# Performance work log

Measured on AMD Instinct MI355X. Metric: run time of the kernel, lower is better.

## Reference

```python
import jax, jax.numpy as jnp
import numpy as np

B, S, IN, H, OUT = 64, 512, 1024, 512, 512
EPS = 1e-5
ADAPTIVE_RATE = 0.01


def setup_inputs() -> dict:
    key = jax.random.key(0)
    ks = iter(jax.random.split(key, 64))

    def rn(shape, scale):
        return (jax.random.normal(next(ks), shape, jnp.float32) * scale)

    d = {}
    d["x"] = jax.random.normal(next(ks), (B, S, IN), jnp.float32)
    d["context"] = jax.random.normal(next(ks), (B, H), jnp.float32)
    d["state_importance"] = jnp.ones((1, H), jnp.float32)
    # embedding
    d["W_emb"], d["b_emb"] = rn((H, IN), 0.02), rn((H,), 0.01)
    # core layers: Linear + BatchNorm1d (gamma=1, beta=0 torch init)
    d["W0"], d["b0"] = rn((H, H), 0.03), rn((H,), 0.01)
    d["g0"], d["bt0"] = jnp.ones((H,), jnp.float32), jnp.zeros((H,), jnp.float32)
    d["W1"], d["b1"] = rn((H, H), 0.03), rn((H,), 0.01)
    d["g1"], d["bt1"] = jnp.ones((H,), jnp.float32), jnp.zeros((H,), jnp.float32)
    # two LSTMCells (hidden -> hidden), torch gate order i,f,g,o
    lstm_scale = 1.0 / np.sqrt(H)
    for l in range(2):
        d[f"Wih{l}"] = rn((4 * H, H), lstm_scale)
        d[f"Whh{l}"] = rn((4 * H, H), lstm_scale)
        d[f"bih{l}"] = rn((4 * H,), lstm_scale)
        d[f"bhh{l}"] = rn((4 * H,), lstm_scale)
    # compression gate: Linear(2H, H) + LayerNorm + Sigmoid
    d["Wc"], d["bc"] = rn((H, 2 * H), 0.02), rn((H,), 0.01)
    d["lnc_g"], d["lnc_b"] = jnp.ones((H,), jnp.float32), jnp.zeros((H,), jnp.float32)
    # importance generator: Linear, ReLU, Linear, LayerNorm, Sigmoid
    d["Wi1"], d["bi1"] = rn((H, H), 0.03), rn((H,), 0.01)
    d["Wi2"], d["bi2"] = rn((H, H), 0.03), rn((H,), 0.01)
    d["lni_g"], d["lni_b"] = jnp.ones((H,), jnp.float32), jnp.zeros((H,), jnp.float32)
    # final layer
    d["Wf"], d["bf"] = rn((OUT, H), 0.03), rn((OUT,), 0.01)
    return d


def _bn_channel_dim1(h, gamma, beta):
    # BatchNorm1d (training mode) on (B, S, H) with channel dim = dim 1 (S == num_features)
    m = h.mean(axis=(0, 2), keepdims=True)
    v = h.var(axis=(0, 2), keepdims=True)  # biased, like torch normalization
    return gamma[None, :, None] * (h - m) / jnp.sqrt(v + EPS) + beta[None, :, None]


def _ln(h, g, b):
    m = h.mean(-1, keepdims=True)
    v = h.var(-1, keepdims=True)
    return g * (h - m) / jnp.sqrt(v + EPS) + b


def _lstm_cell(xt, h, c, Wih, Whh, bih, bhh):
    z = xt @ Wih.T + bih + h @ Whh.T + bhh  # (B, 4H)
    i, f, g, o = jnp.split(z, 4, axis=-1)
    c = jax.nn.sigmoid(f) * c + jax.nn.sigmoid(i) * jnp.tanh(g)
    h = jax.nn.sigmoid(o) * jnp.tanh(c)
    return h, c


def reference(x, context, state_importance, W_emb, b_emb,
              W0, b0, g0, bt0, W1, b1, g1, bt1,
              Wih0, Whh0, bih0, bhh0, Wih1, Whh1, bih1, bhh1,
              Wc, bc, lnc_g, lnc_b, Wi1, bi1, Wi2, bi2, lni_g, lni_b,
              Wf, bf):
    h = x @ W_emb.T + b_emb  # (B, S, H)
    h = jax.nn.relu(_bn_channel_dim1(h @ W0.T + b0, g0, bt0))
    h = jax.nn.relu(_bn_channel_dim1(h @ W1.T + b1, g1, bt1))

    # stacked 2-layer LSTMCell over the sequence, keep only the final hidden
    zeros = jnp.zeros((B, H), h.dtype)

    def step(carry, xt):
        h0, c0, h1, c1 = carry
        h0, c0 = _lstm_cell(xt, h0, c0, Wih0, Whh0, bih0, bhh0)
        h1, c1 = _lstm_cell(h0, h1, c1, Wih1, Whh1, bih1, bhh1)
        return (h0, c0, h1, c1), None

    (h0, c0, h1, c1), _ = jax.lax.scan(step, (zeros, zeros, zeros, zeros),
                                       jnp.swapaxes(h, 0, 1))
    processed = h1  # (B, H)

    comp = jax.nn.sigmoid(_ln(jnp.concatenate([processed, context], axis=-1) @ Wc.T + bc,
                              lnc_g, lnc_b))
    compressed = processed * comp

    imp = jax.nn.sigmoid(_ln(jax.nn.relu(compressed @ Wi1.T + bi1) @ Wi2.T + bi2,
                             lni_g, lni_b))
    si_new = state_importance + ADAPTIVE_RATE * (
        jnp.abs(imp).mean(axis=0, keepdims=True) - state_importance)

    out = compressed @ Wf.T + bf
    return out, si_new
```

## Files before the change

### kernel.cpp

```cpp
#include <hip/hip_runtime.h>
#include <hip/hip_bf16.h>
#include <stdint.h>


typedef __attribute__((ext_vector_type(8))) short short8;
typedef __attribute__((ext_vector_type(4))) float floatx4;
typedef __attribute__((ext_vector_type(4))) unsigned uintx4;

__device__ inline float b2f(short u){
  union { float f; uint32_t i; } x; x.i = ((uint32_t)(uint16_t)u) << 16; return x.f;
}
__device__ inline short f2b(float f){
  union { float f; uint32_t i; } x; x.f = f;
  uint32_t r = (x.i + 0x7FFFu + ((x.i >> 16) & 1u)) >> 16;
  return (short)(uint16_t)r;
}
__device__ inline float sigm(float x){ return 1.0f / (1.0f + __expf(-x)); }

__device__ inline float blk_sum(float v, float* red){
  #pragma unroll
  for (int o = 32; o > 0; o >>= 1) v += __shfl_down(v, o, 64);
  int wv = threadIdx.x >> 6;
  __syncthreads();
  if ((threadIdx.x & 63) == 0) red[wv] = v;
  __syncthreads();
  return red[0] + red[1] + red[2] + red[3];
}

__device__ inline void stage16(const short* g, short* l){
  __builtin_amdgcn_global_load_lds(
      (const __attribute__((address_space(1))) void*)(uintptr_t)g,
      (__attribute__((address_space(3))) void*)(uintptr_t)l,
      16, 0, 0);
}


__global__ void set_flag(const unsigned* __restrict__ si_bits, unsigned* __restrict__ flag){
  if (threadIdx.x == 0 && blockIdx.x == 0)
    *flag = (si_bits[0] == 0x3F800000u) ? 1u : 0u;
}


__global__ __launch_bounds__(256) void convq(
    const unsigned* __restrict__ flag, int mode,
    const void* s0, long e0, short* d0, int n0,
    const void* s1, long e1, short* d1, int n1,
    const void* s2, long e2, short* d2, int n2,
    const void* s3, long e3, short* d3, int n3)
{
  const bool isf32 = (*flag != 0u);
  const int gid = blockIdx.x*256 + threadIdx.x;
  const int stride = gridDim.x*256;
  const void* ss[4] = {s0,s1,s2,s3};
  long ee[4]  = {e0,e1,e2,e3};
  short* dd[4] = {d0,d1,d2,d3};
  int nn[4]   = {n0,n1,n2,n3};
  for (int s = 0; s < 4; s++){
    if (!dd[s]) continue;
    if (mode == 1) {
      if (!isf32) continue;
      for (int i = gid; i < nn[s]; i += stride)
        dd[s][i] = ((const short*)ss[s])[ee[s] + i];
    } else if (isf32) {
      for (int i = gid; i < nn[s]; i += stride)
        dd[s][i] = f2b(((const float*)ss[s])[ee[s] + i]);
    } else {
      for (int i = gid; i < nn[s]; i += stride)
        dd[s][i] = ((const short*)ss[s])[ee[s] + i];
    }
  }
}


__global__ __launch_bounds__(256) void gemm_bt(
    const short* __restrict__ A, const short* __restrict__ A2, int splitRow,
    int lda, const short* __restrict__ W, const short* __restrict__ bias,
    short* __restrict__ C, int ldc, int row0, int K)
{
  __shared__ alignas(16) short As[128*32];
  __shared__ alignas(16) short Bs[128*32];
  const int tid  = threadIdx.x;
  const int lane = tid & 63;
  const int wave = tid >> 6;
  const int wm = wave >> 1, wn = wave & 1;
  const int bm = blockIdx.x, bn = blockIdx.y;
  const int R0 = row0 + bm*128;
  const short* Ab = (R0 < splitRow) ? A2 : A;

  floatx4 acc[4][4];
  #pragma unroll
  for (int i = 0; i < 4; i++)
    #pragma unroll
    for (int j = 0; j < 4; j++){ floatx4 z = {0.f,0.f,0.f,0.f}; acc[i][j] = z; }

  const short* Ag = Ab + (size_t)(R0 + (tid >> 2))*lda + (tid & 3)*8;
  const short* Wg = W  + (size_t)(bn*128 + (tid >> 2))*K + (tid & 3)*8;

  const int kk  = (lane >> 4) * 8;
  const int rA  = wm*64 + (lane & 15);
  const int rB  = wn*64 + (lane & 15);

  for (int k0 = 0; k0 < K; k0 += 32) {
    __syncthreads();
    stage16(Ag + k0,                  As + tid*8);
    stage16(Ag + k0 + (size_t)64*lda, As + 2048 + tid*8);
    stage16(Wg + k0,                  Bs + tid*8);
    stage16(Wg + k0 + (size_t)64*K,   Bs + 2048 + tid*8);
    __syncthreads();

    short8 af[4], bf[4];
    #pragma unroll
    for (int i = 0; i < 4; i++){
      af[i] = *(const short8*)&As[(rA + i*16)*32 + kk];
      bf[i] = *(const short8*)&Bs[(rB + i*16)*32 + kk];
    }
    #pragma unroll
    for (int i = 0; i < 4; i++)
      #pragma unroll
      for (int j = 0; j < 4; j++)
        acc[i][j] = __builtin_amdgcn_mfma_f32_16x16x32_bf16(af[i], bf[j], acc[i][j], 0, 0, 0);
  }

  const int crow0 = R0 + wm*64 + (lane >> 4)*4;
  const int ccol0 = bn*128 + wn*64;
  #pragma unroll
  for (int i = 0; i < 4; i++){
    #pragma unroll
    for (int j = 0; j < 4; j++){
      int col = ccol0 + j*16 + (lane & 15);
      float bv = b2f(bias[col]);
      #pragma unroll
      for (int r = 0; r < 4; r++){
        int row = crow0 + i*16 + r;
        C[(size_t)row*ldc + col] = f2b(acc[i][j][r] + bv);
      }
    }
  }
}


__global__ __launch_bounds__(256) void bn_relu(
    const short* __restrict__ X, const short* __restrict__ gamma,
    const short* __restrict__ beta, short* __restrict__ Y)
{
  const int s = blockIdx.x, tid = threadIdx.x;
  __shared__ float red[4];
  float s1 = 0.f, s2 = 0.f;
  for (int i = tid; i < 4096; i += 256){
    int b = i >> 6, c = i & 63;
    short8 v = *(const short8*)(X + ((size_t)(b*512 + s))*512 + c*8);
    #pragma unroll
    for (int u = 0; u < 8; u++){ float f = b2f(v[u]); s1 += f; s2 += f*f; }
  }
  s1 = blk_sum(s1, red);
  s2 = blk_sum(s2, red);
  float mean = s1 * (1.f/32768.f);
  float var  = fmaxf(s2 * (1.f/32768.f) - mean*mean, 0.f);
  float sc = b2f(gamma[s]) * rsqrtf(var + 1e-5f);
  float sh = b2f(beta[s]) - mean * sc;
  for (int i = tid; i < 4096; i += 256){
    int b = i >> 6, c = i & 63;
    size_t base = ((size_t)(b*512 + s))*512 + c*8;
    short8 v = *(const short8*)(X + base);
    short8 o;
    #pragma unroll
    for (int u = 0; u < 8; u++){
      float f = b2f(v[u]) * sc + sh;
      o[u] = f2b(fmaxf(f, 0.f));
    }
    *(short8*)(Y + base) = o;
  }
}


__global__ __launch_bounds__(256, 1) void lstm_persist(
    const short* __restrict__ Xseq,
    const short* __restrict__ Wih0, const short* __restrict__ Whh0,
    const short* __restrict__ bih0, const short* __restrict__ bhh0,
    const short* __restrict__ Wih1, const short* __restrict__ Whh1,
    const short* __restrict__ bih1, const short* __restrict__ bhh1,
    short* __restrict__ h0r,
    short* __restrict__ h1r,
    unsigned* __restrict__ slots,
    unsigned* __restrict__ epoch)
{
  const int wg   = blockIdx.x;
  const int tid  = threadIdx.x;
  const int lane = tid & 63;
  const int wave = tid >> 6;

  if (wg == 64){
    if (wave != 0) return;
    const unsigned* sp = slots + lane*16;
    unsigned* ep = epoch + lane*16;
    for (unsigned itv = 1; itv <= 512; ++itv){
      for (;;){
        unsigned v;
        asm volatile("global_load_dword %0, %1, off sc1\n\t"
                     "s_waitcnt vmcnt(0)"
                     : "=v"(v) : "v"(sp) : "memory");
        if (__all((int)(v >= itv))) break;
      }
      asm volatile("global_store_dword %0, %1, off sc0 sc1"
                   :: "v"(ep), "v"(itv) : "memory");
    }
    return;
  }

  const int l15  = lane & 15;
  const int quad = lane >> 4;
  const int kq   = quad * 8;

  __shared__ float zp[4*64*33];
  __shared__ unsigned pack[2][256];
  __shared__ alignas(16) short xpf[512];
  #define ZP(t,r,c) zp[((t)*64 + (r))*33 + (c)]

  const short* Wt = (wave==0) ? Wih0 : (wave==1) ? Whh0 : (wave==2) ? Wih1 : Whh1;
  short8 wreg[2][16];
  #pragma unroll
  for (int nt = 0; nt < 2; nt++){
    int g2 = nt*2 + (l15 >> 3);
    int ml = l15 & 7;
    const short* wrow = Wt + (size_t)(g2*512 + wg*8 + ml)*512 + kq;
    #pragma unroll
    for (int kk = 0; kk < 16; kk++)
      wreg[nt][kk] = *(const short8*)(wrow + kk*32);
  }

  const int bb  = tid >> 2;
  const int ml0 = (tid & 3) * 2;
  float bs0[4][2], bs1[4][2];
  #pragma unroll
  for (int g = 0; g < 4; g++)
    #pragma unroll
    for (int p = 0; p < 2; p++){
      int m = wg*8 + ml0 + p;
      bs0[g][p] = b2f(bih0[g*512+m]) + b2f(bhh0[g*512+m]);
      bs1[g][p] = b2f(bih1[g*512+m]) + b2f(bhh1[g*512+m]);
    }
  float c0[2] = {0.f, 0.f}, c1[2] = {0.f, 0.f};

  for (int it = 0; it <= 512; ++it){
    const bool act = (wave==0) ? (it < 512)
                   : (wave==1) ? (it >= 1 && it < 512)
                   : (wave==2) ? (it >= 1)
                   :             (it >= 2);

    if (it > 0 && wave > 0 && act){
      const unsigned want = (unsigned)it;
      const unsigned* ep = epoch + wg*16;
      for (;;){
        unsigned v;
        asm volatile("global_load_dword %0, %1, off sc1\n\t"
                     "s_waitcnt vmcnt(0)"
                     : "=v"(v) : "v"(ep) : "memory");
        if (v >= want) break;
      }
      __builtin_amdgcn_sched_barrier(0);
    }

    floatx4 acc[4][2];
    #pragma unroll
    for (int mt = 0; mt < 4; mt++)
      #pragma unroll
      for (int nt = 0; nt < 2; nt++){ floatx4 z = {0.f,0.f,0.f,0.f}; acc[mt][nt] = z; }

    if (act){
      const short* Ab;
      size_t rstride;
      if (wave == 0)      { Ab = Xseq + (size_t)it*512;               rstride = 262144; }
      else if (wave <= 2) { Ab = h0r + (size_t)((it-1)&1)*32768;      rstride = 512; }
      else                { Ab = h1r + (size_t)(it&1)*32768;          rstride = 512; }
      const short* ap[4];
      #pragma unroll
      for (int mt = 0; mt < 4; mt++)
        ap[mt] = Ab + (size_t)(mt*16 + l15)*rstride + kq;

      if (wave == 0){
        #pragma unroll
        for (int kk = 0; kk < 16; kk++){
          short8 af[4];
          #pragma unroll
          for (int mt = 0; mt < 4; mt++) af[mt] = *(const short8*)(ap[mt] + kk*32);
          #pragma unroll
          for (int mt = 0; mt < 4; mt++){
            acc[mt][0] = __builtin_amdgcn_mfma_f32_16x16x32_bf16(af[mt], wreg[0][kk], acc[mt][0], 0, 0, 0);
            acc[mt][1] = __builtin_amdgcn_mfma_f32_16x16x32_bf16(af[mt], wreg[1][kk], acc[mt][1], 0, 0, 0);
          }
        }
      } else {
        short8 hb[2][4][4];
        #pragma unroll
        for (int pb = 0; pb < 2; pb++)
          #pragma unroll
          for (int kk = 0; kk < 4; kk++)
            #pragma unroll
            for (int mt = 0; mt < 4; mt++)
              asm volatile("global_load_dwordx4 %0, %1, off sc1"
                           : "=v"(hb[pb][kk][mt])
                           : "v"(ap[mt] + (pb*4 + kk)*32));
        #pragma unroll
        for (int kb = 0; kb < 4; kb++){
          const int cur = kb & 1;
          if (kb < 3) asm volatile("s_waitcnt vmcnt(16)" ::: "memory");
          else        asm volatile("s_waitcnt vmcnt(0)"  ::: "memory");
          __builtin_amdgcn_sched_barrier(0);
          #pragma unroll
          for (int kk = 0; kk < 4; kk++)
            #pragma unroll
            for (int mt = 0; mt < 4; mt++){
              acc[mt][0] = __builtin_amdgcn_mfma_f32_16x16x32_bf16(hb[cur][kk][mt], wreg[0][kb*4+kk], acc[mt][0], 0, 0, 0);
              acc[mt][1] = __builtin_amdgcn_mfma_f32_16x16x32_bf16(hb[cur][kk][mt], wreg[1][kb*4+kk], acc[mt][1], 0, 0, 0);
            }
          if (kb < 2){
            #pragma unroll
            for (int kk = 0; kk < 4; kk++)
              #pragma unroll
              for (int mt = 0; mt < 4; mt++)
                asm volatile("global_load_dwordx4 %0, %1, off sc1"
                             : "=v"(hb[cur][kk][mt])
                             : "v"(ap[mt] + ((kb+2)*4 + kk)*32));
          }
        }
      }
    }

    #pragma unroll
    for (int mt = 0; mt < 4; mt++)
      #pragma unroll
      for (int nt = 0; nt < 2; nt++)
        #pragma unroll
        for (int r = 0; r < 4; r++)
          ZP(wave, mt*16 + quad*4 + r, nt*16 + l15) = acc[mt][nt][r];
    __syncthreads();

    if (it < 512){
      float hv[2];
      #pragma unroll
      for (int p = 0; p < 2; p++){
        int ml = ml0 + p;
        float zi = ZP(0, bb,      ml) + ZP(1, bb,      ml) + bs0[0][p];
        float zf = ZP(0, bb,  8 + ml) + ZP(1, bb,  8 + ml) + bs0[1][p];
        float zg = ZP(0, bb, 16 + ml) + ZP(1, bb, 16 + ml) + bs0[2][p];
        float zo = ZP(0, bb, 24 + ml) + ZP(1, bb, 24 + ml) + bs0[3][p];
        c0[p] = sigm(zf)*c0[p] + sigm(zi)*tanhf(zg);
        hv[p] = sigm(zo)*tanhf(c0[p]);
      }
      pack[0][tid] = (unsigned)(uint16_t)f2b(hv[0]) | ((unsigned)(uint16_t)f2b(hv[1]) << 16);
    }
    if (it >= 1){
      float hv[2];
      #pragma unroll
      for (int p = 0; p < 2; p++){
        int ml = ml0 + p;
        float zi = ZP(2, bb,      ml) + ZP(3, bb,      ml) + bs1[0][p];
        float zf = ZP(2, bb,  8 + ml) + ZP(3, bb,  8 + ml) + bs1[1][p];
        float zg = ZP(2, bb, 16 + ml) + ZP(3, bb, 16 + ml) + bs1[2][p];
        float zo = ZP(2, bb, 24 + ml) + ZP(3, bb, 24 + ml) + bs1[3][p];
        c1[p] = sigm(zf)*c1[p] + sigm(zi)*tanhf(zg);
        hv[p] = sigm(zo)*tanhf(c1[p]);
      }
      pack[1][tid] = (unsigned)(uint16_t)f2b(hv[0]) | ((unsigned)(uint16_t)f2b(hv[1]) << 16);
    }
    __syncthreads();

    if (wave == 0 && it < 512){
      uintx4 d = *(const uintx4*)&pack[0][lane*4];
      short* dst = h0r + (size_t)(it&1)*32768 + lane*512 + wg*8;
      asm volatile("global_store_dwordx4 %0, %1, off sc0 sc1" :: "v"(dst), "v"(d) : "memory");
      asm volatile("s_waitcnt vmcnt(0)" ::: "memory");
    }
    if (wave == 1 && it >= 1){
      uintx4 d = *(const uintx4*)&pack[1][lane*4];
      short* dst = h1r + (size_t)((it-1)&1)*32768 + lane*512 + wg*8;
      asm volatile("global_store_dwordx4 %0, %1, off sc0 sc1" :: "v"(dst), "v"(d) : "memory");
      asm volatile("s_waitcnt vmcnt(0)" ::: "memory");
    }
    __syncthreads();
    if (tid == 0){
      unsigned nv = (unsigned)(it + 1);
      asm volatile("global_store_dword %0, %1, off sc0 sc1"
                   :: "v"(slots + wg*16), "v"(nv) : "memory");
    }
    if (wave == 0 && it + 2 < 512){
      const short* nx = Xseq + (size_t)(it + 2)*512 + lane*8;
      #pragma unroll 8
      for (int r = 0; r < 64; ++r)
        stage16(nx + (size_t)r*262144, xpf);
    }
  }
  #undef ZP
}


__global__ __launch_bounds__(256) void head_gate_out(
    const short* __restrict__ h1, const short* __restrict__ ctx,
    const short* __restrict__ Wc, const short* __restrict__ bc,
    const short* __restrict__ lng, const short* __restrict__ lnb,
    const short* __restrict__ Wf, const short* __restrict__ bfb,
    short* __restrict__ compressed, void* __restrict__ outp,
    const unsigned* __restrict__ flag)
{
  const int b = blockIdx.x, tid = threadIdx.x;
  const bool isf32 = (*flag != 0u);
  __shared__ float xc[1024];
  __shared__ float cv[512];
  __shared__ float red[4];
  for (int i = tid; i < 512; i += 256) xc[i]       = b2f(h1 [b*512 + i]);
  for (int i = tid; i < 512; i += 256) xc[512 + i] = b2f(ctx[b*512 + i]);
  __syncthreads();
  float y[2];
  #pragma unroll
  for (int jj = 0; jj < 2; jj++){
    int j = tid + jj*256;
    const short* wr = Wc + (size_t)j*1024;
    float a = 0.f;
    for (int k = 0; k < 1024; k += 8){
      short8 wv = *(const short8*)(wr + k);
      #pragma unroll
      for (int u = 0; u < 8; u++) a += b2f(wv[u]) * xc[k + u];
    }
    y[jj] = a + b2f(bc[j]);
  }
  float s = blk_sum(y[0] + y[1], red);
  float mean = s * (1.f/512.f);
  float q = (y[0]-mean)*(y[0]-mean) + (y[1]-mean)*(y[1]-mean);
  q = blk_sum(q, red);
  float inv = rsqrtf(q * (1.f/512.f) + 1e-5f);
  #pragma unroll
  for (int jj = 0; jj < 2; jj++){
    int j = tid + jj*256;
    float v = (y[jj]-mean)*inv*b2f(lng[j]) + b2f(lnb[j]);
    float cm = xc[j] * sigm(v);
    cv[j] = cm;
    compressed[(size_t)b*512 + j] = f2b(cm);
  }
  __syncthreads();
  #pragma unroll
  for (int jj = 0; jj < 2; jj++){
    int j = tid + jj*256;
    const short* wr = Wf + (size_t)j*512;
    float a = 0.f;
    for (int k = 0; k < 512; k += 8){
      short8 wv = *(const short8*)(wr + k);
      #pragma unroll
      for (int u = 0; u < 8; u++) a += b2f(wv[u]) * cv[k + u];
    }
    float o = a + b2f(bfb[j]);
    if (isf32) ((float*)outp)[(size_t)b*512 + j] = o;
    else       ((short*)outp)[(size_t)b*512 + j] = f2b(o);
  }
}


__global__ __launch_bounds__(256) void head_imp(
    const short* __restrict__ compressed,
    const short* __restrict__ Wi1, const short* __restrict__ bi1,
    const short* __restrict__ Wi2, const short* __restrict__ bi2,
    const short* __restrict__ lng, const short* __restrict__ lnb,
    float* __restrict__ imp)
{
  const int b = blockIdx.x, tid = threadIdx.x;
  __shared__ float xr[512];
  __shared__ float t1[512];
  __shared__ float red[4];
  for (int i = tid; i < 512; i += 256) xr[i] = b2f(compressed[b*512 + i]);
  __syncthreads();
  #pragma unroll
  for (int jj = 0; jj < 2; jj++){
    int j = tid + jj*256;
    const short* wr = Wi1 + (size_t)j*512;
    float a = 0.f;
    for (int k = 0; k < 512; k += 8){
      short8 wv = *(const short8*)(wr + k);
      #pragma unroll
      for (int u = 0; u < 8; u++) a += b2f(wv[u]) * xr[k + u];
    }
    t1[j] = fmaxf(a + b2f(bi1[j]), 0.f);
  }
  __syncthreads();
  float y[2];
  #pragma unroll
  for (int jj = 0; jj < 2; jj++){
    int j = tid + jj*256;
    const short* wr = Wi2 + (size_t)j*512;
    float a = 0.f;
    for (int k = 0; k < 512; k += 8){
      short8 wv = *(const short8*)(wr + k);
      #pragma unroll
      for (int u = 0; u < 8; u++) a += b2f(wv[u]) * t1[k + u];
    }
    y[jj] = a + b2f(bi2[j]);
  }
  float s = blk_sum(y[0] + y[1], red);
  float mean = s * (1.f/512.f);
  float q = (y[0]-mean)*(y[0]-mean) + (y[1]-mean)*(y[1]-mean);
  q = blk_sum(q, red);
  float inv = rsqrtf(q * (1.f/512.f) + 1e-5f);
  #pragma unroll
  for (int jj = 0; jj < 2; jj++){
    int j = tid + jj*256;
    imp[(size_t)b*512 + j] = sigm((y[jj]-mean)*inv*b2f(lng[j]) + b2f(lnb[j]));
  }
}


__global__ __launch_bounds__(256) void head_si(
    const float* __restrict__ imp, const short* __restrict__ si,
    void* __restrict__ outp, const unsigned* __restrict__ flag)
{
  int tid = threadIdx.x;
  const bool isf32 = (*flag != 0u);
  #pragma unroll
  for (int mm = 0; mm < 2; mm++){
    int m = tid + mm*256;
    float s = 0.f;
    for (int b = 0; b < 64; b++) s += fabsf(imp[(size_t)b*512 + m]);
    float mean = s * (1.f/64.f);
    float sv = b2f(si[m]);
    float o = sv + 0.01f*(mean - sv);
    if (isf32) ((float*)outp)[32768 + m] = o;
    else       ((short*)outp)[32768 + m] = f2b(o);
  }
}


extern "C" void kernel_launch(void* const* d_in, const int* in_sizes, int n_in,
                              void* d_out, int out_size, void* d_ws, size_t ws_size,
                              hipStream_t stream)
{
  (void)in_sizes; (void)n_in; (void)out_size; (void)ws_size;
  char* ws = (char*)d_ws;
  unsigned* slots  = (unsigned*)(ws);
  unsigned* epoch  = (unsigned*)(ws + 4096);
  unsigned* flag   = (unsigned*)(ws + 8192);
  short*    xStage = (short*)(ws + 12288);
  short*    ring   = (short*)(ws + 274432);
  short*    comp   = (short*)(ws + 798720);
  float*    impb   = (float*)(ws + 864256);
  short*    SA     = (short*)(ws + 995328);

  short* h0r = ring;
  short* h1r = ring + 65536;

  short* aWemb = SA + 0;
  short* aW0   = SA + 524288;
  short* aW1   = SA + 786432;
  short* aWih0 = SA + 1048576;
  short* aWhh0 = SA + 2097152;
  short* aWih1 = SA + 3145728;
  short* aWhh1 = SA + 4194304;
  short* aWc   = SA + 5242880;
  short* aWi1  = SA + 5767168;
  short* aWi2  = SA + 6029312;
  short* aWf   = SA + 6291456;
  short* V     = SA + 6553600;
  short* abemb = V + 0;     short* ab0  = V + 512;   short* ag0  = V + 1024;
  short* abt0  = V + 1536;  short* ab1  = V + 2048;  short* ag1  = V + 2560;
  short* abt1  = V + 3072;  short* abih0= V + 3584;  short* abhh0= V + 5632;
  short* abih1 = V + 7680;  short* abhh1= V + 9728;  short* abc  = V + 11776;
  short* alncg = V + 12288; short* alncb= V + 12800; short* abi1 = V + 13312;
  short* abi2  = V + 13824; short* alnig= V + 14336; short* alnib= V + 14848;
  short* abfb  = V + 15360; short* actx = V + 15872; short* asi  = V + 48640;

  short* xb  = (short*)d_in[0];
  short* hL0 = xb + 16777216;

  hipMemsetAsync(slots, 0, 8192, stream);
  set_flag<<<1, 64, 0, stream>>>((const unsigned*)d_in[2], flag);

  dim3 blk(256);
  convq<<<256, blk, 0, stream>>>(flag, 0,
      d_in[0], 0, xStage, 65536, nullptr,0,nullptr,0, nullptr,0,nullptr,0, nullptr,0,nullptr,0);
  for (long n0 = 65536; n0 < 33554432; n0 <<= 1) {
    int blocks = (int)((n0 + 1023) / 1024); if (blocks > 4096) blocks = 4096;
    convq<<<blocks, blk, 0, stream>>>(flag, 0,
        d_in[0], n0, xb + n0, (int)n0, nullptr,0,nullptr,0, nullptr,0,nullptr,0, nullptr,0,nullptr,0);
  }
  convq<<<64, blk, 0, stream>>>(flag, 1,
      xStage, 0, xb, 65536, nullptr,0,nullptr,0, nullptr,0,nullptr,0, nullptr,0,nullptr,0);

  convq<<<1024, blk, 0, stream>>>(flag, 0,
      d_in[3], 0, aWemb, 524288,  d_in[5], 0, aW0, 262144,
      d_in[9], 0, aW1,   262144,  d_in[21],0, aWc, 524288);
  convq<<<2048, blk, 0, stream>>>(flag, 0,
      d_in[13],0, aWih0, 1048576, d_in[14],0, aWhh0, 1048576,
      d_in[17],0, aWih1, 1048576, d_in[18],0, aWhh1, 1048576);
  convq<<<1024, blk, 0, stream>>>(flag, 0,
      d_in[25],0, aWi1, 262144,   d_in[27],0, aWi2, 262144,
      d_in[31],0, aWf,  262144,   d_in[1], 0, actx, 32768);
  convq<<<8, blk, 0, stream>>>(flag, 0,
      d_in[4], 0, abemb, 512,  d_in[6], 0, ab0, 512,
      d_in[7], 0, ag0,   512,  d_in[8], 0, abt0, 512);
  convq<<<8, blk, 0, stream>>>(flag, 0,
      d_in[10],0, ab1, 512,  d_in[11],0, ag1, 512,
      d_in[12],0, abt1,512,  d_in[22],0, abc, 512);
  convq<<<8, blk, 0, stream>>>(flag, 0,
      d_in[15],0, abih0, 2048,  d_in[16],0, abhh0, 2048,
      d_in[19],0, abih1, 2048,  d_in[20],0, abhh1, 2048);
  convq<<<8, blk, 0, stream>>>(flag, 0,
      d_in[23],0, alncg, 512,  d_in[24],0, alncb, 512,
      d_in[26],0, abi1,  512,  d_in[28],0, abi2,  512);
  convq<<<8, blk, 0, stream>>>(flag, 0,
      d_in[29],0, alnig, 512,  d_in[30],0, alnib, 512,
      d_in[32],0, abfb,  512,  d_in[2], 0, asi,   512);

  gemm_bt<<<dim3(1, 4), blk, 0, stream>>>(xb, xb, 0, 1024, aWemb, abemb,
                                          xStage, 512, 0, 1024);
  for (int r0 = 128; r0 < 32768; r0 <<= 1) {
    gemm_bt<<<dim3(r0/128, 4), blk, 0, stream>>>(xb, xb, 0, 1024, aWemb, abemb,
                                                 xb, 512, r0, 1024);
  }
  gemm_bt<<<dim3(256, 4), blk, 0, stream>>>(xb, xStage, 128, 512, aW0, ab0,
                                            hL0, 512, 0, 512);
  bn_relu<<<512, blk, 0, stream>>>(hL0, ag0, abt0, hL0);
  gemm_bt<<<dim3(256, 4), blk, 0, stream>>>(hL0, hL0, 0, 512, aW1, ab1,
                                            xb, 512, 0, 512);
  bn_relu<<<512, blk, 0, stream>>>(xb, ag1, abt1, xb);

  lstm_persist<<<65, blk, 0, stream>>>(xb, aWih0, aWhh0, abih0, abhh0,
                                       aWih1, aWhh1, abih1, abhh1,
                                       h0r, h1r, slots, epoch);

  head_gate_out<<<64, blk, 0, stream>>>(h1r + 32768, actx, aWc, abc, alncg, alncb,
                                        aWf, abfb, comp, d_out, flag);
  head_imp<<<64, blk, 0, stream>>>(comp, aWi1, abi1, aWi2, abi2, alnig, alnib, impb);
  head_si<<<1, blk, 0, stream>>>(impb, asi, d_out, flag);
}
```

Measured before the change: 7.044 ms.

## Split LSTM layer barriers into independent per-layer flags with LDS wave signaling

```diff
diff --git a/kernel.cpp b/kernel.cpp
--- a/kernel.cpp
+++ b/kernel.cpp
@@ -5,7 +5,7 @@
 
 typedef __attribute__((ext_vector_type(8))) short short8;
 typedef __attribute__((ext_vector_type(4))) float floatx4;
-typedef __attribute__((ext_vector_type(4))) unsigned uintx4;
+typedef __attribute__((ext_vector_type(2))) unsigned uintx2;
 
 __device__ inline float b2f(short u){
   union { float f; uint32_t i; } x; x.i = ((uint32_t)(uint16_t)u) << 16; return x.f;
@@ -32,6 +32,16 @@
       (const __attribute__((address_space(1))) void*)(uintptr_t)g,
       (__attribute__((address_space(3))) void*)(uintptr_t)l,
       16, 0, 0);
+}
+
+__device__ inline int ldsLoadAcq(int* p){
+  return __hip_atomic_load(p, __ATOMIC_ACQUIRE, __HIP_MEMORY_SCOPE_WORKGROUP);
+}
+__device__ inline void ldsStoreRel(int* p, int v){
+  __hip_atomic_store(p, v, __ATOMIC_RELEASE, __HIP_MEMORY_SCOPE_WORKGROUP);
+}
+__device__ inline int ldsAddRel(int* p){
+  return __hip_atomic_fetch_add(p, 1, __ATOMIC_RELEASE, __HIP_MEMORY_SCOPE_WORKGROUP);
 }
 
 
@@ -181,8 +191,10 @@
     const short* __restrict__ bih1, const short* __restrict__ bhh1,
     short* __restrict__ h0r,
     short* __restrict__ h1r,
-    unsigned* __restrict__ slots,
-    unsigned* __restrict__ epoch)
+    unsigned* __restrict__ f0,
+    unsigned* __restrict__ f1,
+    unsigned* __restrict__ ep0,
+    unsigned* __restrict__ ep1)
 {
   const int wg   = blockIdx.x;
   const int tid  = threadIdx.x;
@@ -190,9 +202,9 @@
   const int wave = tid >> 6;
 
   if (wg == 64){
-    if (wave != 0) return;
-    const unsigned* sp = slots + lane*16;
-    unsigned* ep = epoch + lane*16;
+    if (wave >= 2) return;
+    const unsigned* sp = (wave == 0 ? f0 : f1) + lane*16;
+    unsigned* dp = (wave == 0 ? ep0 : ep1) + lane*16;
     for (unsigned itv = 1; itv <= 512; ++itv){
       for (;;){
         unsigned v;
@@ -202,7 +214,7 @@
         if (__all((int)(v >= itv))) break;
       }
       asm volatile("global_store_dword %0, %1, off sc0 sc1"
-                   :: "v"(ep), "v"(itv) : "memory");
+                   :: "v"(dp), "v"(itv) : "memory");
     }
     return;
   }
@@ -211,10 +223,15 @@
   const int quad = lane >> 4;
   const int kq   = quad * 8;
 
-  __shared__ float zp[4*64*33];
-  __shared__ unsigned pack[2][256];
+  __shared__ float zp0[2*2*64*33];
+  __shared__ float zp1[2*2*64*33];
   __shared__ alignas(16) short xpf[512];
-  #define ZP(t,r,c) zp[((t)*64 + (r))*33 + (c)]
+  __shared__ int go0, go1, zc0, zc1, gc0, gc1;
+  #define ZPL0(p,t,r,c) zp0[((((p)*2+(t))*64) + (r))*33 + (c)]
+  #define ZPL1(p,t,r,c) zp1[((((p)*2+(t))*64) + (r))*33 + (c)]
+
+  if (tid == 0){ go0 = -1; go1 = -1; zc0 = 0; zc1 = 0; gc0 = 0; gc1 = 0; }
+  __syncthreads();
 
   const short* Wt = (wave==0) ? Wih0 : (wave==1) ? Whh0 : (wave==2) ? Wih1 : Whh1;
   short8 wreg[2][16];
@@ -228,18 +245,21 @@
       wreg[nt][kk] = *(const short8*)(wrow + kk*32);
   }
 
-  const int bb  = tid >> 2;
-  const int ml0 = (tid & 3) * 2;
-  float bs0[4][2], bs1[4][2];
+  const int lp  = wave >> 1;
+  const int t2  = tid & 127;
+  const int bbg = t2 >> 1;
+  const int m4  = (t2 & 1) * 4;
+  const short* biA = lp ? bih1 : bih0;
+  const short* bhA = lp ? bhh1 : bhh0;
+  float bsL[4][4];
   #pragma unroll
   for (int g = 0; g < 4; g++)
     #pragma unroll
-    for (int p = 0; p < 2; p++){
-      int m = wg*8 + ml0 + p;
-      bs0[g][p] = b2f(bih0[g*512+m]) + b2f(bhh0[g*512+m]);
-      bs1[g][p] = b2f(bih1[g*512+m]) + b2f(bhh1[g*512+m]);
-    }
-  float c0[2] = {0.f, 0.f}, c1[2] = {0.f, 0.f};
+    for (int j = 0; j < 4; j++){
+      int m = wg*8 + m4 + j;
+      bsL[g][j] = b2f(biA[g*512+m]) + b2f(bhA[g*512+m]);
+    }
+  float cst[4] = {0.f, 0.f, 0.f, 0.f};
 
   for (int it = 0; it <= 512; ++it){
     const bool act = (wave==0) ? (it < 512)
@@ -247,16 +267,36 @@
                    : (wave==2) ? (it >= 1)
                    :             (it >= 2);
 
-    if (it > 0 && wave > 0 && act){
+    if (wave == 1 && it >= 1){
       const unsigned want = (unsigned)it;
-      const unsigned* ep = epoch + wg*16;
+      const unsigned* p = ep0 + wg*16;
       for (;;){
         unsigned v;
         asm volatile("global_load_dword %0, %1, off sc1\n\t"
                      "s_waitcnt vmcnt(0)"
-                     : "=v"(v) : "v"(ep) : "memory");
+                     : "=v"(v) : "v"(p) : "memory");
         if (v >= want) break;
       }
+      __builtin_amdgcn_sched_barrier(0);
+      if (lane == 0) ldsStoreRel(&go0, it);
+    }
+    if (wave == 3){
+      if (it >= 2){
+        const unsigned want = (unsigned)it;
+        const unsigned* p = ep1 + wg*16;
+        for (;;){
+          unsigned v;
+          asm volatile("global_load_dword %0, %1, off sc1\n\t"
+                       "s_waitcnt vmcnt(0)"
+                       : "=v"(v) : "v"(p) : "memory");
+          if (v >= want) break;
+        }
+        __builtin_amdgcn_sched_barrier(0);
+      }
+      if (lane == 0) ldsStoreRel(&go1, it);
+    }
+    if (wave == 2 && it >= 1){
+      while (ldsLoadAcq(&go0) < it) { }
       __builtin_amdgcn_sched_barrier(0);
     }
 
@@ -326,71 +366,104 @@
       }
     }
 
-    #pragma unroll
-    for (int mt = 0; mt < 4; mt++)
-      #pragma unroll
-      for (int nt = 0; nt < 2; nt++)
+    const int par = it & 1;
+    if (wave < 2){
+      if (it < 512){
+        if (it >= 2) while (ldsLoadAcq(&gc0) < 2*(it-1)) { }
         #pragma unroll
-        for (int r = 0; r < 4; r++)
-          ZP(wave, mt*16 + quad*4 + r, nt*16 + l15) = acc[mt][nt][r];
-    __syncthreads();
-
-    if (it < 512){
-      float hv[2];
-      #pragma unroll
-      for (int p = 0; p < 2; p++){
-        int ml = ml0 + p;
-        float zi = ZP(0, bb,      ml) + ZP(1, bb,      ml) + bs0[0][p];
-        float zf = ZP(0, bb,  8 + ml) + ZP(1, bb,  8 + ml) + bs0[1][p];
-        float zg = ZP(0, bb, 16 + ml) + ZP(1, bb, 16 + ml) + bs0[2][p];
-        float zo = ZP(0, bb, 24 + ml) + ZP(1, bb, 24 + ml) + bs0[3][p];
-        c0[p] = sigm(zf)*c0[p] + sigm(zi)*tanhf(zg);
-        hv[p] = sigm(zo)*tanhf(c0[p]);
-      }
-      pack[0][tid] = (unsigned)(uint16_t)f2b(hv[0]) | ((unsigned)(uint16_t)f2b(hv[1]) << 16);
-    }
-    if (it >= 1){
-      float hv[2];
-      #pragma unroll
-      for (int p = 0; p < 2; p++){
-        int ml = ml0 + p;
-        float zi = ZP(2, bb,      ml) + ZP(3, bb,      ml) + bs1[0][p];
-        float zf = ZP(2, bb,  8 + ml) + ZP(3, bb,  8 + ml) + bs1[1][p];
-        float zg = ZP(2, bb, 16 + ml) + ZP(3, bb, 16 + ml) + bs1[2][p];
-        float zo = ZP(2, bb, 24 + ml) + ZP(3, bb, 24 + ml) + bs1[3][p];
-        c1[p] = sigm(zf)*c1[p] + sigm(zi)*tanhf(zg);
-        hv[p] = sigm(zo)*tanhf(c1[p]);
-      }
-      pack[1][tid] = (unsigned)(uint16_t)f2b(hv[0]) | ((unsigned)(uint16_t)f2b(hv[1]) << 16);
-    }
-    __syncthreads();
-
-    if (wave == 0 && it < 512){
-      uintx4 d = *(const uintx4*)&pack[0][lane*4];
-      short* dst = h0r + (size_t)(it&1)*32768 + lane*512 + wg*8;
-      asm volatile("global_store_dwordx4 %0, %1, off sc0 sc1" :: "v"(dst), "v"(d) : "memory");
-      asm volatile("s_waitcnt vmcnt(0)" ::: "memory");
-    }
-    if (wave == 1 && it >= 1){
-      uintx4 d = *(const uintx4*)&pack[1][lane*4];
-      short* dst = h1r + (size_t)((it-1)&1)*32768 + lane*512 + wg*8;
-      asm volatile("global_store_dwordx4 %0, %1, off sc0 sc1" :: "v"(dst), "v"(d) : "memory");
-      asm volatile("s_waitcnt vmcnt(0)" ::: "memory");
-    }
-    __syncthreads();
-    if (tid == 0){
-      unsigned nv = (unsigned)(it + 1);
-      asm volatile("global_store_dword %0, %1, off sc0 sc1"
-                   :: "v"(slots + wg*16), "v"(nv) : "memory");
-    }
-    if (wave == 0 && it + 2 < 512){
-      const short* nx = Xseq + (size_t)(it + 2)*512 + lane*8;
-      #pragma unroll 8
-      for (int r = 0; r < 64; ++r)
-        stage16(nx + (size_t)r*262144, xpf);
-    }
-  }
-  #undef ZP
+        for (int mt = 0; mt < 4; mt++)
+          #pragma unroll
+          for (int nt = 0; nt < 2; nt++)
+            #pragma unroll
+            for (int r = 0; r < 4; r++)
+              ZPL0(par, wave, mt*16 + quad*4 + r, nt*16 + l15) = acc[mt][nt][r];
+        if (lane == 0) ldsAddRel(&zc0);
+      }
+    } else {
+      if (it >= 1){
+        if (it >= 3) while (ldsLoadAcq(&gc1) < 2*(it-2)) { }
+        #pragma unroll
+        for (int mt = 0; mt < 4; mt++)
+          #pragma unroll
+          for (int nt = 0; nt < 2; nt++)
+            #pragma unroll
+            for (int r = 0; r < 4; r++)
+              ZPL1(par, wave-2, mt*16 + quad*4 + r, nt*16 + l15) = acc[mt][nt][r];
+        if (lane == 0) ldsAddRel(&zc1);
+      }
+    }
+
+    if (wave < 2){
+      if (it < 512){
+        while (ldsLoadAcq(&zc0) < 2*(it+1)) { }
+        if (it >= 2) while (ldsLoadAcq(&go1) < it) { }
+        float hv[4];
+        #pragma unroll
+        for (int j = 0; j < 4; j++){
+          int ml = m4 + j;
+          float zi = ZPL0(par,0,bbg,      ml) + ZPL0(par,1,bbg,      ml) + bsL[0][j];
+          float zf = ZPL0(par,0,bbg,  8 + ml) + ZPL0(par,1,bbg,  8 + ml) + bsL[1][j];
+          float zg = ZPL0(par,0,bbg, 16 + ml) + ZPL0(par,1,bbg, 16 + ml) + bsL[2][j];
+          float zo = ZPL0(par,0,bbg, 24 + ml) + ZPL0(par,1,bbg, 24 + ml) + bsL[3][j];
+          cst[j] = sigm(zf)*cst[j] + sigm(zi)*tanhf(zg);
+          hv[j] = sigm(zo)*tanhf(cst[j]);
+        }
+        uintx2 d;
+        d.x = (unsigned)(uint16_t)f2b(hv[0]) | ((unsigned)(uint16_t)f2b(hv[1]) << 16);
+        d.y = (unsigned)(uint16_t)f2b(hv[2]) | ((unsigned)(uint16_t)f2b(hv[3]) << 16);
+        short* dst = h0r + (size_t)par*32768 + bbg*512 + wg*8 + m4;
+        asm volatile("global_store_dwordx2 %0, %1, off sc0 sc1" :: "v"(dst), "v"(d) : "memory");
+        asm volatile("s_waitcnt vmcnt(0)" ::: "memory");
+        __builtin_amdgcn_sched_barrier(0);
+        if (lane == 0){
+          int old = ldsAddRel(&gc0);
+          if (old == 2*it + 1){
+            unsigned nv = (unsigned)(it + 1);
+            asm volatile("global_store_dword %0, %1, off sc0 sc1"
+                         :: "v"(f0 + wg*16), "v"(nv) : "memory");
+          }
+        }
+      }
+      if (wave == 0 && it + 2 < 512){
+        const short* nx = Xseq + (size_t)(it + 2)*512 + lane*8;
+        #pragma unroll 8
+        for (int r = 0; r < 64; ++r)
+          stage16(nx + (size_t)r*262144, xpf);
+      }
+    } else {
+      if (it >= 1){
+        while (ldsLoadAcq(&zc1) < 2*it) { }
+        float hv[4];
+        #pragma unroll
+        for (int j = 0; j < 4; j++){
+          int ml = m4 + j;
+          float zi = ZPL1(par,0,bbg,      ml) + ZPL1(par,1,bbg,      ml) + bsL[0][j];
+          float zf = ZPL1(par,0,bbg,  8 + ml) + ZPL1(par,1,bbg,  8 + ml) + bsL[1][j];
+          float zg = ZPL1(par,0,bbg, 16 + ml) + ZPL1(par,1,bbg, 16 + ml) + bsL[2][j];
+          float zo = ZPL1(par,0,bbg, 24 + ml) + ZPL1(par,1,bbg, 24 + ml) + bsL[3][j];
+          cst[j] = sigm(zf)*cst[j] + sigm(zi)*tanhf(zg);
+          hv[j] = sigm(zo)*tanhf(cst[j]);
+        }
+        uintx2 d;
+        d.x = (unsigned)(uint16_t)f2b(hv[0]) | ((unsigned)(uint16_t)f2b(hv[1]) << 16);
+        d.y = (unsigned)(uint16_t)f2b(hv[2]) | ((unsigned)(uint16_t)f2b(hv[3]) << 16);
+        short* dst = h1r + (size_t)((it-1)&1)*32768 + bbg*512 + wg*8 + m4;
+        asm volatile("global_store_dwordx2 %0, %1, off sc0 sc1" :: "v"(dst), "v"(d) : "memory");
+        asm volatile("s_waitcnt vmcnt(0)" ::: "memory");
+        __builtin_amdgcn_sched_barrier(0);
+        if (lane == 0){
+          int old = ldsAddRel(&gc1);
+          if (old == 2*it - 1){
+            unsigned nv = (unsigned)(it + 1);
+            asm volatile("global_store_dword %0, %1, off sc0 sc1"
+                         :: "v"(f1 + wg*16), "v"(nv) : "memory");
+          }
+        }
+      }
+    }
+  }
+  #undef ZPL0
+  #undef ZPL1
 }
 
 
@@ -532,14 +605,16 @@
 {
   (void)in_sizes; (void)n_in; (void)out_size; (void)ws_size;
   char* ws = (char*)d_ws;
-  unsigned* slots  = (unsigned*)(ws);
-  unsigned* epoch  = (unsigned*)(ws + 4096);
-  unsigned* flag   = (unsigned*)(ws + 8192);
-  short*    xStage = (short*)(ws + 12288);
-  short*    ring   = (short*)(ws + 274432);
-  short*    comp   = (short*)(ws + 798720);
-  float*    impb   = (float*)(ws + 864256);
-  short*    SA     = (short*)(ws + 995328);
+  unsigned* f0b    = (unsigned*)(ws);
+  unsigned* f1b    = (unsigned*)(ws + 4096);
+  unsigned* ep0b   = (unsigned*)(ws + 8192);
+  unsigned* ep1b   = (unsigned*)(ws + 12288);
+  unsigned* flag   = (unsigned*)(ws + 16384);
+  short*    xStage = (short*)(ws + 20480);
+  short*    ring   = (short*)(ws + 282624);
+  short*    comp   = (short*)(ws + 806912);
+  float*    impb   = (float*)(ws + 872448);
+  short*    SA     = (short*)(ws + 1003520);
 
   short* h0r = ring;
   short* h1r = ring + 65536;
@@ -567,7 +642,7 @@
   short* xb  = (short*)d_in[0];
   short* hL0 = xb + 16777216;
 
-  hipMemsetAsync(slots, 0, 8192, stream);
+  hipMemsetAsync(ws, 0, 16384, stream);
   set_flag<<<1, 64, 0, stream>>>((const unsigned*)d_in[2], flag);
 
   dim3 blk(256);
@@ -621,7 +696,7 @@
 
   lstm_persist<<<65, blk, 0, stream>>>(xb, aWih0, aWhh0, abih0, abhh0,
                                        aWih1, aWhh1, abih1, abhh1,
-                                       h0r, h1r, slots, epoch);
+                                       h0r, h1r, f0b, f1b, ep0b, ep1b);
 
   head_gate_out<<<64, blk, 0, stream>>>(h1r + 32768, actx, aWc, abc, alncg, alncb,
                                         aWf, abfb, comp, d_out, flag);
```

Result: faster. 6.796 ms (-3.5%).
